# Performance work log

Hardware: AMD Instinct MI355X
Metric: run time of the kernel (lower is better)

The kernel has to match this reference:

```python
import jax, jax.numpy as jnp
import numpy as np

BLOCK_SIZE = 256
N_EMBD = 256
HEAD_SIZE = 64


def setup_inputs() -> dict:
    key = jax.random.key(0)
    k1, k2, k3, k4, k5 = jax.random.split(key, 5)
    B, T = 256, 256
    x = jax.random.normal(k1, (B, T, N_EMBD), dtype=jnp.float32)
    # nn.Linear(n_embd, head_size, bias=False) weights, stored as [in, out] for x @ W
    s = 1.0 / np.sqrt(N_EMBD)
    Wk = jax.random.uniform(k2, (N_EMBD, HEAD_SIZE), minval=-s, maxval=s, dtype=jnp.float32)
    Wq = jax.random.uniform(k3, (N_EMBD, HEAD_SIZE), minval=-s, maxval=s, dtype=jnp.float32)
    Wv = jax.random.uniform(k4, (N_EMBD, HEAD_SIZE), minval=-s, maxval=s, dtype=jnp.float32)
    rel_pos_embedding = 0.02 * jax.random.normal(k5, (2 * BLOCK_SIZE - 1, HEAD_SIZE), dtype=jnp.float32)
    return {"x": x, "Wk": Wk, "Wq": Wq, "Wv": Wv, "rel_pos_embedding": rel_pos_embedding}


def reference(x, Wk, Wq, Wv, rel_pos_embedding):
    B, T, C = x.shape
    H = Wk.shape[-1]
    k = x @ Wk  # [B,T,H]
    q = x @ Wq  # [B,T,H]
    v = x @ Wv  # [B,T,H]
    # content scores (scaled); note: position scores are NOT scaled, matching original
    content = jnp.einsum('bth,bsh->bts', q, k) * (H ** -0.5)  # [B,T,T]
    # relative position indices: j - i + (block_size - 1)
    idx = jnp.arange(T)[None, :] - jnp.arange(T)[:, None] + (BLOCK_SIZE - 1)  # [T,T]
    rel_emb = rel_pos_embedding[idx]  # [T,T,H]
    position = jnp.einsum('bth,tsh->bts', q, rel_emb)  # [B,T,T]
    wei = content + position
    causal = jnp.tril(jnp.ones((T, T), dtype=bool))
    wei = jnp.where(causal[None, :, :], wei, -jnp.inf)
    wei = jax.nn.softmax(wei, axis=-1)
    # dropout omitted (eval mode / deterministic reference)
    out = jnp.einsum('bts,bsh->bth', wei, v)  # [B,T,H]
    return out
```

## Files before the change

kernel.cpp:

```cpp
#include <hip/hip_runtime.h>

#define BB 256
#define TT 256
#define CC 256
#define HH 64

typedef _Float16 half8 __attribute__((ext_vector_type(8)));
typedef _Float16 half4 __attribute__((ext_vector_type(4)));
typedef __fp16 fp16x2 __attribute__((ext_vector_type(2)));
typedef float floatx4 __attribute__((ext_vector_type(4)));

__global__ __launch_bounds__(512) void fused(
    const float* __restrict__ x,
    const float* __restrict__ Wk, const float* __restrict__ Wq, const float* __restrict__ Wv,
    const float* __restrict__ rpe,
    _Float16* __restrict__ qh, _Float16* __restrict__ kh, _Float16* __restrict__ vTh,
    float* __restrict__ out)
{
    __shared__ __align__(16) unsigned char ldsbuf[96 * 1024];
    __shared__ _Float16 rpeS[256 * 72];
    _Float16* wt = (_Float16*)ldsbuf;

    const int tid  = threadIdx.x;
    const int b    = blockIdx.x;
    const int w    = tid >> 6;
    const int lane = tid & 63;
    const int quad = lane >> 4;
    const int l    = lane & 15;

    {
        const float* Ws[3] = {Wk, Wq, Wv};
#pragma unroll
        for (int wsel = 0; wsel < 3; ++wsel) {
            const float4* W4 = reinterpret_cast<const float4*>(Ws[wsel]);
#pragma unroll
            for (int j = 0; j < 8; ++j) {
                const int f4 = tid + j * 512;
                const float4 v = W4[f4];
                const int k  = f4 >> 4;
                const int n0 = (f4 & 15) * 4;
                const int g  = k >> 3;
                const int ke = k & 7;
#pragma unroll
                for (int e = 0; e < 4; ++e) {
                    const int row = wsel * 64 + n0 + e;
                    const int pg  = g ^ (row & 31);
                    wt[row * 256 + pg * 8 + ke] = (_Float16)((&v.x)[e]);
                }
            }
        }
        const float4* R4 = reinterpret_cast<const float4*>(rpe);
#pragma unroll
        for (int j = 0; j < 8; ++j) {
            const int f4 = tid + j * 512;
            const float4 v = R4[f4];
            const int r  = f4 >> 4;
            const int h0 = (f4 & 15) * 4;
            half4 hv;
            hv[0] = (_Float16)v.x; hv[1] = (_Float16)v.y;
            hv[2] = (_Float16)v.z; hv[3] = (_Float16)v.w;
            *(half4*)&rpeS[r * 72 + h0] = hv;
        }
    }
    __syncthreads();

    {
        const int row0 = b * 256 + w * 32;
        floatx4 acc[12][2];
#pragma unroll
        for (int nt = 0; nt < 12; ++nt)
#pragma unroll
            for (int rt = 0; rt < 2; ++rt) acc[nt][rt] = (floatx4){0.f, 0.f, 0.f, 0.f};

        const float4* xg = reinterpret_cast<const float4*>(x);
        union H8 { half8 v; fp16x2 p[4]; };

#pragma unroll
        for (int kk = 0; kk < 8; ++kk) {
            const size_t base0 = (size_t)(row0 + l) * 64 + kk * 8 + quad * 2;
            const size_t base1 = base0 + 16 * 64;
            const float4 a0lo = xg[base0], a0hi = xg[base0 + 1];
            const float4 a1lo = xg[base1], a1hi = xg[base1 + 1];
            H8 u0, u1;
            u0.p[0] = __builtin_amdgcn_cvt_pkrtz(a0lo.x, a0lo.y);
            u0.p[1] = __builtin_amdgcn_cvt_pkrtz(a0lo.z, a0lo.w);
            u0.p[2] = __builtin_amdgcn_cvt_pkrtz(a0hi.x, a0hi.y);
            u0.p[3] = __builtin_amdgcn_cvt_pkrtz(a0hi.z, a0hi.w);
            u1.p[0] = __builtin_amdgcn_cvt_pkrtz(a1lo.x, a1lo.y);
            u1.p[1] = __builtin_amdgcn_cvt_pkrtz(a1lo.z, a1lo.w);
            u1.p[2] = __builtin_amdgcn_cvt_pkrtz(a1hi.x, a1hi.y);
            u1.p[3] = __builtin_amdgcn_cvt_pkrtz(a1hi.z, a1hi.w);

#pragma unroll
            for (int nt = 0; nt < 12; ++nt) {
                const int row = nt * 16 + l;
                const int pg  = (kk * 4 + quad) ^ (row & 31);
                const half8 bf = *(const half8*)&wt[row * 256 + pg * 8];
                acc[nt][0] = __builtin_amdgcn_mfma_f32_16x16x32_f16(u0.v, bf, acc[nt][0], 0, 0, 0);
                acc[nt][1] = __builtin_amdgcn_mfma_f32_16x16x32_f16(u1.v, bf, acc[nt][1], 0, 0, 0);
            }
        }

        const int trw = w * 32;
#pragma unroll
        for (int nt = 0; nt < 4; ++nt) {
#pragma unroll
            for (int rt = 0; rt < 2; ++rt) {
#pragma unroll
                for (int r = 0; r < 4; ++r) {
                    const size_t row = (size_t)row0 + rt * 16 + quad * 4 + r;
                    kh[row * HH + nt * 16 + l] = (_Float16)(acc[nt][rt][r] * 0.125f);
                    qh[row * HH + nt * 16 + l] = (_Float16)acc[nt + 4][rt][r];
                }
                half4 vv;
                vv[0] = (_Float16)acc[nt + 8][rt][0];
                vv[1] = (_Float16)acc[nt + 8][rt][1];
                vv[2] = (_Float16)acc[nt + 8][rt][2];
                vv[3] = (_Float16)acc[nt + 8][rt][3];
                *(half4*)(vTh + ((size_t)b * HH + nt * 16 + l) * TT + trw + rt * 16 + quad * 4) = vv;
            }
        }
    }
    __syncthreads();

    _Float16* wh = (_Float16*)ldsbuf + w * (16 * 264);

#pragma unroll
    for (int pass = 0; pass < 2; ++pass) {
        const int tile  = pass ? (15 - w) : w;
        const int tw    = tile * 16;
        const int stmax = tile;
        const int cmax  = tile >> 1;
        const int dtmin = 15 - tile;

        const _Float16* qp = qh + (size_t)(b * TT + tw + l) * HH + quad * 8;
        const half8 qf0 = *(const half8*)qp;
        const half8 qf1 = *(const half8*)(qp + 32);

#pragma unroll
        for (int dt = 0; dt < 16; ++dt) {
            if (dt >= dtmin) {
                const _Float16* rp = &rpeS[(dt * 16 + l) * 72 + quad * 8];
                const half8 bf0 = *(const half8*)rp;
                const half8 bf1 = *(const half8*)(rp + 32);
                floatx4 z = {0.f, 0.f, 0.f, 0.f};
                z = __builtin_amdgcn_mfma_f32_16x16x32_f16(qf0, bf0, z, 0, 0, 0);
                const floatx4 pacc = __builtin_amdgcn_mfma_f32_16x16x32_f16(qf1, bf1, z, 0, 0, 0);
                if (dt == dtmin) {
#pragma unroll
                    for (int r = 0; r < 4; ++r) {
                        const int row = quad * 4 + r;
                        const int s   = l + row - 15;
                        if (s >= 0) wh[row * 264 + s] = (_Float16)pacc[r];
                    }
                } else {
#pragma unroll
                    for (int r = 0; r < 4; ++r) {
                        const int row = quad * 4 + r;
                        const int s   = dt * 16 + l + tw + row - 255;
                        wh[row * 264 + s] = (_Float16)pacc[r];
                    }
                }
            }
        }

        floatx4 sacc[16];
#pragma unroll
        for (int st = 0; st < 16; ++st) {
            if (st <= stmax) {
                const _Float16* kp = kh + (size_t)(b * TT + st * 16 + l) * HH + quad * 8;
                const half8 kf0 = *(const half8*)kp;
                const half8 kf1 = *(const half8*)(kp + 32);
                floatx4 z = {0.f, 0.f, 0.f, 0.f};
                z = __builtin_amdgcn_mfma_f32_16x16x32_f16(qf0, kf0, z, 0, 0, 0);
                sacc[st] = __builtin_amdgcn_mfma_f32_16x16x32_f16(qf1, kf1, z, 0, 0, 0);
            }
        }

        float sums[4] = {0.f, 0.f, 0.f, 0.f};
#pragma unroll
        for (int st = 0; st < 16; ++st) {
            if (st < stmax) {
                const int s = l + 16 * st;
#pragma unroll
                for (int r = 0; r < 4; ++r) {
                    const int row = quad * 4 + r;
                    const float e = __expf(sacc[st][r] + (float)wh[row * 264 + s]);
                    sums[r] += e;
                    wh[row * 264 + s] = (_Float16)e;
                }
            }
        }
        {
            const int s = l + 16 * stmax;
#pragma unroll
            for (int r = 0; r < 4; ++r) {
                const int row = quad * 4 + r;
                float e = 0.f;
                if (l <= row) e = __expf(sacc[stmax][r] + (float)wh[row * 264 + s]);
                sums[r] += e;
                wh[row * 264 + s] = (_Float16)e;
            }
        }
        if ((tile & 1) == 0) {
            const int s = l + 16 * (stmax + 1);
#pragma unroll
            for (int r = 0; r < 4; ++r) wh[(quad * 4 + r) * 264 + s] = (_Float16)0.f;
        }

        float inv_r[4];
#pragma unroll
        for (int r = 0; r < 4; ++r) {
            float sum = sums[r];
            sum += __shfl_xor(sum, 1);
            sum += __shfl_xor(sum, 2);
            sum += __shfl_xor(sum, 4);
            sum += __shfl_xor(sum, 8);
            inv_r[r] = 1.0f / sum;
        }

        floatx4 oacc[4] = {{0.f,0.f,0.f,0.f},{0.f,0.f,0.f,0.f},
                           {0.f,0.f,0.f,0.f},{0.f,0.f,0.f,0.f}};
#pragma unroll
        for (int c = 0; c < 8; ++c) {
            if (c <= cmax) {
                const half8 af = *(const half8*)&wh[l * 264 + c * 32 + quad * 8];
#pragma unroll
                for (int ht = 0; ht < 4; ++ht) {
                    const half8 vf = *(const half8*)(vTh +
                        ((size_t)b * HH + ht * 16 + l) * TT + c * 32 + quad * 8);
                    oacc[ht] = __builtin_amdgcn_mfma_f32_16x16x32_f16(af, vf, oacc[ht], 0, 0, 0);
                }
            }
        }

#pragma unroll
        for (int ht = 0; ht < 4; ++ht) {
#pragma unroll
            for (int r = 0; r < 4; ++r) {
                const int t = tw + quad * 4 + r;
                out[(size_t)(b * TT + t) * HH + ht * 16 + l] = oacc[ht][r] * inv_r[r];
            }
        }
    }
}

extern "C" void kernel_launch(void* const* d_in, const int* in_sizes, int n_in,
                              void* d_out, int out_size, void* d_ws, size_t ws_size,
                              hipStream_t stream) {
    const float* x   = (const float*)d_in[0];
    const float* Wk  = (const float*)d_in[1];
    const float* Wq  = (const float*)d_in[2];
    const float* Wv  = (const float*)d_in[3];
    const float* rpe = (const float*)d_in[4];
    float* out = (float*)d_out;

    const size_t NQ = (size_t)BB * TT * HH;
    _Float16* qh  = (_Float16*)d_ws;
    _Float16* kh  = qh + NQ;
    _Float16* vTh = kh + NQ;

    fused<<<dim3(BB), dim3(512), 0, stream>>>(x, Wk, Wq, Wv, rpe, qh, kh, vTh, out);
}
```

Before: 142.7 us.

## Shrink LDS footprint to raise occupancy: chunk weight staging, read rel-pos from global

The LDS buffer drops from about 96KB plus a rel-pos table to about 67KB. The weights for the QKV projection are now staged in two K-chunks with unswizzled padded rows. The relative-position embedding is no longer staged in LDS; it is loaded from global memory and converted to fp16 at each use. Launch bounds now request more blocks per CU, trading extra global loads, conversions and a barrier per chunk for higher occupancy and latency hiding.

```diff
diff --git a/kernel.cpp b/kernel.cpp
--- a/kernel.cpp
+++ b/kernel.cpp
@@ -10,15 +10,14 @@
 typedef __fp16 fp16x2 __attribute__((ext_vector_type(2)));
 typedef float floatx4 __attribute__((ext_vector_type(4)));
 
-__global__ __launch_bounds__(512) void fused(
+__global__ __launch_bounds__(512, 4) void fused(
     const float* __restrict__ x,
     const float* __restrict__ Wk, const float* __restrict__ Wq, const float* __restrict__ Wv,
     const float* __restrict__ rpe,
     _Float16* __restrict__ qh, _Float16* __restrict__ kh, _Float16* __restrict__ vTh,
     float* __restrict__ out)
 {
-    __shared__ __align__(16) unsigned char ldsbuf[96 * 1024];
-    __shared__ _Float16 rpeS[256 * 72];
+    __shared__ __align__(16) unsigned char ldsbuf[8 * 16 * 264 * 2];
     _Float16* wt = (_Float16*)ldsbuf;
 
     const int tid  = threadIdx.x;
@@ -28,56 +27,38 @@
     const int quad = lane >> 4;
     const int l    = lane & 15;
 
-    {
-        const float* Ws[3] = {Wk, Wq, Wv};
+    union H8 { half8 v; fp16x2 p[4]; };
+    const float* Ws[3] = {Wk, Wq, Wv};
+    const float4* xg = reinterpret_cast<const float4*>(x);
+
+    const int row0 = b * 256 + w * 32;
+    floatx4 acc[12][2];
+#pragma unroll
+    for (int nt = 0; nt < 12; ++nt)
+#pragma unroll
+        for (int rt = 0; rt < 2; ++rt) acc[nt][rt] = (floatx4){0.f, 0.f, 0.f, 0.f};
+
+#pragma unroll
+    for (int c = 0; c < 2; ++c) {
 #pragma unroll
         for (int wsel = 0; wsel < 3; ++wsel) {
             const float4* W4 = reinterpret_cast<const float4*>(Ws[wsel]);
 #pragma unroll
-            for (int j = 0; j < 8; ++j) {
-                const int f4 = tid + j * 512;
-                const float4 v = W4[f4];
-                const int k  = f4 >> 4;
-                const int n0 = (f4 & 15) * 4;
-                const int g  = k >> 3;
-                const int ke = k & 7;
-#pragma unroll
-                for (int e = 0; e < 4; ++e) {
-                    const int row = wsel * 64 + n0 + e;
-                    const int pg  = g ^ (row & 31);
-                    wt[row * 256 + pg * 8 + ke] = (_Float16)((&v.x)[e]);
-                }
-            }
-        }
-        const float4* R4 = reinterpret_cast<const float4*>(rpe);
-#pragma unroll
-        for (int j = 0; j < 8; ++j) {
-            const int f4 = tid + j * 512;
-            const float4 v = R4[f4];
-            const int r  = f4 >> 4;
-            const int h0 = (f4 & 15) * 4;
-            half4 hv;
-            hv[0] = (_Float16)v.x; hv[1] = (_Float16)v.y;
-            hv[2] = (_Float16)v.z; hv[3] = (_Float16)v.w;
-            *(half4*)&rpeS[r * 72 + h0] = hv;
-        }
-    }
-    __syncthreads();
-
-    {
-        const int row0 = b * 256 + w * 32;
-        floatx4 acc[12][2];
-#pragma unroll
-        for (int nt = 0; nt < 12; ++nt)
-#pragma unroll
-            for (int rt = 0; rt < 2; ++rt) acc[nt][rt] = (floatx4){0.f, 0.f, 0.f, 0.f};
-
-        const float4* xg = reinterpret_cast<const float4*>(x);
-        union H8 { half8 v; fp16x2 p[4]; };
-
-#pragma unroll
-        for (int kk = 0; kk < 8; ++kk) {
-            const size_t base0 = (size_t)(row0 + l) * 64 + kk * 8 + quad * 2;
+            for (int j = 0; j < 4; ++j) {
+                const int f4   = tid + j * 512;
+                const int kloc = f4 >> 4;
+                const int n0   = (f4 & 15) * 4;
+                const float4 v = W4[(size_t)(c * 128 + kloc) * 16 + (f4 & 15)];
+#pragma unroll
+                for (int e = 0; e < 4; ++e)
+                    wt[(wsel * 64 + n0 + e) * 136 + kloc] = (_Float16)((&v.x)[e]);
+            }
+        }
+        __syncthreads();
+
+#pragma unroll
+        for (int kk = 0; kk < 4; ++kk) {
+            const size_t base0 = (size_t)(row0 + l) * 64 + c * 32 + kk * 8 + quad * 2;
             const size_t base1 = base0 + 16 * 64;
             const float4 a0lo = xg[base0], a0hi = xg[base0 + 1];
             const float4 a1lo = xg[base1], a1hi = xg[base1 + 1];
@@ -93,14 +74,15 @@
 
 #pragma unroll
             for (int nt = 0; nt < 12; ++nt) {
-                const int row = nt * 16 + l;
-                const int pg  = (kk * 4 + quad) ^ (row & 31);
-                const half8 bf = *(const half8*)&wt[row * 256 + pg * 8];
+                const half8 bf = *(const half8*)&wt[(nt * 16 + l) * 136 + kk * 32 + quad * 8];
                 acc[nt][0] = __builtin_amdgcn_mfma_f32_16x16x32_f16(u0.v, bf, acc[nt][0], 0, 0, 0);
                 acc[nt][1] = __builtin_amdgcn_mfma_f32_16x16x32_f16(u1.v, bf, acc[nt][1], 0, 0, 0);
             }
         }
-
+        __syncthreads();
+    }
+
+    {
         const int trw = w * 32;
 #pragma unroll
         for (int nt = 0; nt < 4; ++nt) {
@@ -124,6 +106,7 @@
     __syncthreads();
 
     _Float16* wh = (_Float16*)ldsbuf + w * (16 * 264);
+    const float4* rp4 = reinterpret_cast<const float4*>(rpe);
 
 #pragma unroll
     for (int pass = 0; pass < 2; ++pass) {
@@ -140,12 +123,21 @@
 #pragma unroll
         for (int dt = 0; dt < 16; ++dt) {
             if (dt >= dtmin) {
-                const _Float16* rp = &rpeS[(dt * 16 + l) * 72 + quad * 8];
-                const half8 bf0 = *(const half8*)rp;
-                const half8 bf1 = *(const half8*)(rp + 32);
+                const size_t rb = (size_t)(dt * 16 + l) * 16 + quad * 2;
+                const float4 r0lo = rp4[rb],     r0hi = rp4[rb + 1];
+                const float4 r1lo = rp4[rb + 8], r1hi = rp4[rb + 9];
+                H8 v0, v1;
+                v0.p[0] = __builtin_amdgcn_cvt_pkrtz(r0lo.x, r0lo.y);
+                v0.p[1] = __builtin_amdgcn_cvt_pkrtz(r0lo.z, r0lo.w);
+                v0.p[2] = __builtin_amdgcn_cvt_pkrtz(r0hi.x, r0hi.y);
+                v0.p[3] = __builtin_amdgcn_cvt_pkrtz(r0hi.z, r0hi.w);
+                v1.p[0] = __builtin_amdgcn_cvt_pkrtz(r1lo.x, r1lo.y);
+                v1.p[1] = __builtin_amdgcn_cvt_pkrtz(r1lo.z, r1lo.w);
+                v1.p[2] = __builtin_amdgcn_cvt_pkrtz(r1hi.x, r1hi.y);
+                v1.p[3] = __builtin_amdgcn_cvt_pkrtz(r1hi.z, r1hi.w);
                 floatx4 z = {0.f, 0.f, 0.f, 0.f};
-                z = __builtin_amdgcn_mfma_f32_16x16x32_f16(qf0, bf0, z, 0, 0, 0);
-                const floatx4 pacc = __builtin_amdgcn_mfma_f32_16x16x32_f16(qf1, bf1, z, 0, 0, 0);
+                z = __builtin_amdgcn_mfma_f32_16x16x32_f16(qf0, v0.v, z, 0, 0, 0);
+                const floatx4 pacc = __builtin_amdgcn_mfma_f32_16x16x32_f16(qf1, v1.v, z, 0, 0, 0);
                 if (dt == dtmin) {
 #pragma unroll
                     for (int r = 0; r < 4; ++r) {
```

New measurement: 187.0 us. +31.0%, slower.
